# Performance work log

Measured on AMD Instinct MI355X. Metric: run time of the kernel, lower is better.

The kernel has to match this reference:

```python
import jax, jax.numpy as jnp
import numpy as np


def setup_inputs() -> dict:
    key = jax.random.key(0)
    k1, k2, k3, k4, k5, k6 = jax.random.split(key, 6)
    B, S, I, H = 64, 512, 1024, 1024
    scale_ih = 1.0 / np.sqrt(I)
    scale_hh = 1.0 / np.sqrt(H)
    return {
        "inputs": jax.random.normal(k1, (B, S, I), dtype=jnp.float32),
        "h0": jax.random.normal(k2, (1, B, H), dtype=jnp.float32),
        "weight_ih": jax.random.normal(k3, (H, I), dtype=jnp.float32) * scale_ih,
        "weight_hh": jax.random.normal(k4, (H, H), dtype=jnp.float32) * scale_hh,
        "bias_ih": jax.random.normal(k5, (H,), dtype=jnp.float32) * 0.01,
        "bias_hh": jax.random.normal(k6, (H,), dtype=jnp.float32) * 0.01,
    }


def reference(inputs, h0, weight_ih, weight_hh, bias_ih, bias_hh):
    # Elman RNN with ReLU: h_t = relu(x_t W_ih^T + b_ih + h_{t-1} W_hh^T + b_hh)
    # inputs: [B, S, I]; h0: [1, B, H]
    # Precompute the input projection for all timesteps in one big GEMM.
    x_proj = jnp.einsum('bsi,hi->bsh', inputs, weight_ih) + bias_ih + bias_hh  # [B,S,H]

    def step(h, xp_t):
        h_new = jax.nn.relu(xp_t + jnp.matmul(h, weight_hh.T))  # [B,H]
        return h_new, h_new

    h_init = h0[0]  # [B, H]
    h_last, outs = jax.lax.scan(step, h_init, jnp.swapaxes(x_proj, 0, 1))  # outs: [S,B,H]
    outputs = jnp.swapaxes(outs, 0, 1)  # [B, S, H]
    h_n = h_last[None]  # [1, B, H]
    return outputs, h_n
```

## Files before the change

kernel.cpp:

```cpp
#include <hip/hip_runtime.h>
#include <hip/hip_bf16.h>
#include <stdint.h>

#define BATCH 64
#define SEQ   512
#define INDIM 1024
#define HDIM  1024
#define NBLK  256
#define NGRP  8
#define GSLOT 32
#define FPAD  16
#define GBUF_U16 32768
#define GBUF_DW  16384

typedef short bf16x8 __attribute__((ext_vector_type(8)));
typedef short s16x4  __attribute__((ext_vector_type(4)));
typedef float f32x4  __attribute__((ext_vector_type(4)));
typedef unsigned short u16;
typedef unsigned int   u32;
typedef u32 u32x4 __attribute__((ext_vector_type(4)));
typedef u16 u16x4 __attribute__((ext_vector_type(4)));

static __device__ __forceinline__ u16 f2bf(float x) {
  unsigned int u = __float_as_uint(x);
  u += 0x7fffu + ((u >> 16) & 1u);
  return (u16)(u >> 16);
}
static __device__ __forceinline__ float bf2f(u16 b) {
  return __uint_as_float(((unsigned int)b) << 16);
}

static __device__ __forceinline__ int coh_ld_i32(const int* p) {
  int v;
  asm volatile("global_load_dword %0, %1, off sc0 sc1\n\t"
               "s_waitcnt vmcnt(0)"
               : "=&v"(v) : "v"(p) : "memory");
  return v;
}

static __device__ __forceinline__ void split4(float4 v, u16x4& hi, u16x4& lo) {
  hi.x = f2bf(v.x); lo.x = f2bf(v.x - bf2f(hi.x));
  hi.y = f2bf(v.y); lo.y = f2bf(v.y - bf2f(hi.y));
  hi.z = f2bf(v.z); lo.z = f2bf(v.z - bf2f(hi.z));
  hi.w = f2bf(v.w); lo.w = f2bf(v.w - bf2f(hi.w));
}
static __device__ __forceinline__ bf16x8 ld8(const u16* p) {
  s16x4 a = *(const s16x4*)p;
  s16x4 b = *(const s16x4*)(p + 4);
  return __builtin_shufflevector(a, b, 0, 1, 2, 3, 4, 5, 6, 7);
}

__global__ void init0(int* __restrict__ flags, int n) {
  int i = blockIdx.x * blockDim.x + threadIdx.x;
  if (i < n) flags[i] = 0;
}

__global__ void init1(const float* __restrict__ h0, u32* __restrict__ hw) {
  int i = blockIdx.x * blockDim.x + threadIdx.x;
  if (i < BATCH * HDIM) {
    int b = i >> 10, k = i & 1023;
    int g = b >> 3, r = b & 7;
    int k32 = k >> 5, kg = (k >> 3) & 3, j = k & 7;
    float x = h0[i];
    u16 hi = f2bf(x);
    u16 lo = f2bf(x - bf2f(hi));
    size_t di = (size_t)g * (2 * GBUF_DW) + (size_t)((k32 * 64 + kg * 16 + r) * 8 + j);
    hw[di] = (u32)hi | ((u32)lo << 16);
  }
}

__global__ __launch_bounds__(256) void xproj_kernel(const float* __restrict__ A,
                                                    const float* __restrict__ W,
                                                    const float* __restrict__ bih,
                                                    const float* __restrict__ bhh,
                                                    float* __restrict__ C) {
  __shared__ u16 Ah[4][128][12], Al[4][128][12], Bh[4][128][12], Bl[4][128][12];
  const int nb = blockIdx.x;
  const int mb = blockIdx.y;
  const int m_base = mb * 128, n_base = nb * 128;
  const int tid = (int)threadIdx.x;
  const int wid = tid >> 6, lane = tid & 63;
  const int wm = wid >> 1, wn = wid & 1;
  const int r = lane & 15, kg = lane >> 4;
  const int srow = tid >> 1;
  const int skq  = (tid & 1) * 16;

  const float* ap0 = A + (size_t)(m_base + srow) * INDIM + skq;
  const float* bp0 = W + (size_t)(n_base + srow) * INDIM + skq;

  f32x4 acc[4][4] = {};

  for (int k0 = 0; k0 < INDIM; k0 += 32) {
    float4 av[4], bv[4];
#pragma unroll
    for (int i = 0; i < 4; ++i) {
      av[i] = *(const float4*)(ap0 + k0 + i * 4);
      bv[i] = *(const float4*)(bp0 + k0 + i * 4);
    }
    __syncthreads();
#pragma unroll
    for (int i = 0; i < 4; ++i) {
      int kk = skq + i * 4;
      int kgw = kk >> 3, off = kk & 7;
      u16x4 hi, lo;
      split4(av[i], hi, lo);
      *(u16x4*)&Ah[kgw][srow][off] = hi;
      *(u16x4*)&Al[kgw][srow][off] = lo;
      split4(bv[i], hi, lo);
      *(u16x4*)&Bh[kgw][srow][off] = hi;
      *(u16x4*)&Bl[kgw][srow][off] = lo;
    }
    __syncthreads();

    bf16x8 ah[4], al[4], bhv[4], blv[4];
#pragma unroll
    for (int mf = 0; mf < 4; ++mf) {
      int row = wm * 64 + mf * 16 + r;
      ah[mf] = ld8(&Ah[kg][row][0]);
      al[mf] = ld8(&Al[kg][row][0]);
    }
#pragma unroll
    for (int nf = 0; nf < 4; ++nf) {
      int row = wn * 64 + nf * 16 + r;
      bhv[nf] = ld8(&Bh[kg][row][0]);
      blv[nf] = ld8(&Bl[kg][row][0]);
    }
#pragma unroll
    for (int mf = 0; mf < 4; ++mf)
#pragma unroll
      for (int nf = 0; nf < 4; ++nf) {
        acc[mf][nf] = __builtin_amdgcn_mfma_f32_16x16x32_bf16(ah[mf], bhv[nf], acc[mf][nf], 0, 0, 0);
        acc[mf][nf] = __builtin_amdgcn_mfma_f32_16x16x32_bf16(ah[mf], blv[nf], acc[mf][nf], 0, 0, 0);
        acc[mf][nf] = __builtin_amdgcn_mfma_f32_16x16x32_bf16(al[mf], bhv[nf], acc[mf][nf], 0, 0, 0);
      }
  }

#pragma unroll
  for (int nf = 0; nf < 4; ++nf) {
    int col = n_base + wn * 64 + nf * 16 + r;
    float bias = bih[col] + bhh[col];
#pragma unroll
    for (int mf = 0; mf < 4; ++mf) {
      int rowb = m_base + wm * 64 + mf * 16 + kg * 4;
#pragma unroll
      for (int q = 0; q < 4; ++q) {
        C[(size_t)(rowb + q) * HDIM + col] = acc[mf][nf][q] + bias;
      }
    }
  }
}

__global__ __launch_bounds__(576, 1) void rnn_scan(
    const float* __restrict__ Whh, float* __restrict__ out,
    u16* hbase, int* flags) {
  __shared__ u16 WH[32][2][64][8], WL[32][2][64][8];
  __shared__ __align__(16) float red[2][8][2][8][20];
  __shared__ __align__(16) float xfbuf[2][8][32];
  __shared__ __align__(16) float sbuf[2][8][32];

  const int blk = (int)blockIdx.x;
  const int grp = blk & 7;
  const int slot = blk >> 3;
  const int n0 = slot * 32;
  const int tid = (int)threadIdx.x;
  const int wv = tid >> 6, lane = tid & 63;
  const int r = lane & 15, kg = lane >> 4;
  const bool zrow = r >= 8;

  for (int f4 = tid; f4 < 8192; f4 += 576) {
    int row = f4 >> 8;
    int k0 = (f4 & 255) * 4;
    float4 v = *(const float4*)(Whh + (size_t)(n0 + row) * HDIM + k0);
    int k32 = k0 >> 5, kgg = (k0 >> 3) & 3, j = k0 & 7;
    int nt = row >> 4, ln = kgg * 16 + (row & 15);
    u16x4 hi, lo;
    split4(v, hi, lo);
    *(u16x4*)&WH[k32][nt][ln][j] = hi;
    *(u16x4*)&WL[k32][nt][ln][j] = lo;
  }
  __syncthreads();

  u16* const hb0 = hbase + (size_t)grp * (2 * GBUF_U16);
  u16* const hb1 = hb0 + GBUF_U16;
  int* const gflag = flags + grp * GSLOT * FPAD;
  const int* const pollp = gflag + ((wv & 7) * 4 + (lane & 3)) * FPAD;

  const int erow = lane >> 3;
  const int ec4 = (lane & 7) * 4;
  float* const xpp = out + ((size_t)(grp * 8 + erow) * SEQ) * HDIM + n0 + ec4;

  for (int t = 0; t < SEQ; ++t) {
    const int p2 = t & 1;

    if (wv < 8) {
      const u16* hc = (t & 1) ? hb1 : hb0;

      if (t > 0) {
        int v;
        do { v = coh_ld_i32(pollp); } while (!__all(v >= t));
      }

      u32x4 P0, P1, P2, P3, P4, P5, P6, P7;
      if (!zrow) {
        const char* a0 = (const char*)hc + (size_t)((wv * 4) * 64 + lane) * 32;
        const char* a1 = a0 + 4096;
        asm volatile(
            "global_load_dwordx4 %0, %8, off sc0 sc1\n\t"
            "global_load_dwordx4 %1, %8, off offset:16 sc0 sc1\n\t"
            "global_load_dwordx4 %2, %8, off offset:2048 sc0 sc1\n\t"
            "global_load_dwordx4 %3, %8, off offset:2064 sc0 sc1\n\t"
            "global_load_dwordx4 %4, %9, off sc0 sc1\n\t"
            "global_load_dwordx4 %5, %9, off offset:16 sc0 sc1\n\t"
            "global_load_dwordx4 %6, %9, off offset:2048 sc0 sc1\n\t"
            "global_load_dwordx4 %7, %9, off offset:2064 sc0 sc1"
            : "=&v"(P0), "=&v"(P1), "=&v"(P2), "=&v"(P3),
              "=&v"(P4), "=&v"(P5), "=&v"(P6), "=&v"(P7)
            : "v"(a0), "v"(a1)
            : "memory");
        asm volatile("s_waitcnt vmcnt(0)"
            : "+v"(P0), "+v"(P1), "+v"(P2), "+v"(P3),
              "+v"(P4), "+v"(P5), "+v"(P6), "+v"(P7));
      } else {
        P0 = P1 = P2 = P3 = P4 = P5 = P6 = P7 = (u32x4){0, 0, 0, 0};
      }

      f32x4 acc0 = {0.f, 0.f, 0.f, 0.f};
      f32x4 acc1 = {0.f, 0.f, 0.f, 0.f};
#define DO_K32(i, QA, QB)                                                      \
      {                                                                        \
        u32 d0 = QA[0], d1 = QA[1], d2 = QA[2], d3 = QA[3];                    \
        u32 d4 = QB[0], d5 = QB[1], d6 = QB[2], d7 = QB[3];                    \
        union { u32 w[4]; bf16x8 v; } AH, AL;                                  \
        AH.w[0] = (d0 & 0xFFFFu) | (d1 << 16);                                 \
        AH.w[1] = (d2 & 0xFFFFu) | (d3 << 16);                                 \
        AH.w[2] = (d4 & 0xFFFFu) | (d5 << 16);                                 \
        AH.w[3] = (d6 & 0xFFFFu) | (d7 << 16);                                 \
        AL.w[0] = (d0 >> 16) | (d1 & 0xFFFF0000u);                             \
        AL.w[1] = (d2 >> 16) | (d3 & 0xFFFF0000u);                             \
        AL.w[2] = (d4 >> 16) | (d5 & 0xFFFF0000u);                             \
        AL.w[3] = (d6 >> 16) | (d7 & 0xFFFF0000u);                             \
        int k32 = wv * 4 + (i);                                                \
        bf16x8 b0h = *(const bf16x8*)&WH[k32][0][lane][0];                     \
        bf16x8 b0l = *(const bf16x8*)&WL[k32][0][lane][0];                     \
        bf16x8 b1h = *(const bf16x8*)&WH[k32][1][lane][0];                     \
        bf16x8 b1l = *(const bf16x8*)&WL[k32][1][lane][0];                     \
        acc0 = __builtin_amdgcn_mfma_f32_16x16x32_bf16(AH.v, b0h, acc0, 0, 0, 0); \
        acc0 = __builtin_amdgcn_mfma_f32_16x16x32_bf16(AH.v, b0l, acc0, 0, 0, 0); \
        acc0 = __builtin_amdgcn_mfma_f32_16x16x32_bf16(AL.v, b0h, acc0, 0, 0, 0); \
        acc1 = __builtin_amdgcn_mfma_f32_16x16x32_bf16(AH.v, b1h, acc1, 0, 0, 0); \
        acc1 = __builtin_amdgcn_mfma_f32_16x16x32_bf16(AH.v, b1l, acc1, 0, 0, 0); \
        acc1 = __builtin_amdgcn_mfma_f32_16x16x32_bf16(AL.v, b1h, acc1, 0, 0, 0); \
      }
      DO_K32(0, P0, P1)
      DO_K32(1, P2, P3)
      DO_K32(2, P4, P5)
      DO_K32(3, P6, P7)
#undef DO_K32

      if (kg < 2) {
#pragma unroll
        for (int q = 0; q < 4; ++q) {
          red[p2][wv][0][kg * 4 + q][r] = acc0[q];
          red[p2][wv][1][kg * 4 + q][r] = acc1[q];
        }
      }
      __syncthreads();

      if (wv == 0) {
        f32x4 s = *(const f32x4*)&xfbuf[p2][erow][ec4];
        const int nt = ec4 >> 4, cl = ec4 & 15;
#pragma unroll
        for (int w = 0; w < 8; ++w) s += *(const f32x4*)&red[p2][w][nt][erow][cl];
#pragma unroll
        for (int j = 0; j < 4; ++j) s[j] = s[j] > 0.f ? s[j] : 0.f;
        *(f32x4*)&sbuf[p2][erow][ec4] = s;

        u32x4 D;
#pragma unroll
        for (int j = 0; j < 4; ++j) {
          u16 hi = f2bf(s[j]);
          u16 lo = f2bf(s[j] - bf2f(hi));
          D[j] = (u32)hi | ((u32)lo << 16);
        }
        u16* hnx = (t & 1) ? hb0 : hb1;
        u32* hp = (u32*)hnx + (size_t)((slot * 64 + (ec4 >> 3) * 16 + erow) * 8 + (ec4 & 7));
        asm volatile("global_store_dwordx4 %0, %1, off sc1\n\t"
                     "s_waitcnt vmcnt(0)"
                     :: "v"(hp), "v"(D) : "memory");
        if (lane == 0) {
          int* fp = gflag + slot * FPAD;
          int tv = t + 1;
          asm volatile("global_store_dword %0, %1, off sc0 sc1"
                       :: "v"(fp), "v"(tv) : "memory");
        }
      }
    } else {
      if (t >= 2) {
        f32x4 sv = *(const f32x4*)&sbuf[p2][erow][ec4];
        __builtin_nontemporal_store(sv, (f32x4*)(xpp + (size_t)(t - 2) * HDIM));
      }
      float4 xv = *(const float4*)(xpp + (size_t)t * HDIM);
      f32x4 xr = {xv.x, xv.y, xv.z, xv.w};
      *(f32x4*)&xfbuf[p2][erow][ec4] = xr;
      __syncthreads();
    }
  }

  __syncthreads();
  if (wv == 8) {
    f32x4 s2 = *(const f32x4*)&sbuf[(SEQ - 2) & 1][erow][ec4];
    __builtin_nontemporal_store(s2, (f32x4*)(xpp + (size_t)(SEQ - 2) * HDIM));
    f32x4 s1 = *(const f32x4*)&sbuf[(SEQ - 1) & 1][erow][ec4];
    __builtin_nontemporal_store(s1, (f32x4*)(xpp + (size_t)(SEQ - 1) * HDIM));
  }
}

__global__ void copy_hn(const float* __restrict__ out, float* __restrict__ hn) {
  int idx = blockIdx.x * blockDim.x + threadIdx.x;
  if (idx < BATCH * HDIM) {
    int b = idx >> 10, j = idx & 1023;
    hn[idx] = out[((size_t)b * SEQ + (SEQ - 1)) * (size_t)HDIM + j];
  }
}

extern "C" void kernel_launch(void* const* d_in, const int* in_sizes, int n_in,
                              void* d_out, int out_size, void* d_ws, size_t ws_size,
                              hipStream_t stream) {
  const float* inputs = (const float*)d_in[0];
  const float* h0     = (const float*)d_in[1];
  const float* w_ih   = (const float*)d_in[2];
  const float* w_hh   = (const float*)d_in[3];
  const float* b_ih   = (const float*)d_in[4];
  const float* b_hh   = (const float*)d_in[5];

  float* outBase = (float*)d_out;
  float* hnBase  = outBase + (size_t)BATCH * SEQ * HDIM;

  u16* hbase = (u16*)d_ws;
  int* flags = (int*)(hbase + (size_t)NGRP * 2 * GBUF_U16);
  const int nflags = NGRP * GSLOT * FPAD;

  init0<<<(nflags + 255) / 256, 256, 0, stream>>>(flags, nflags);
  init1<<<(BATCH * HDIM + 255) / 256, 256, 0, stream>>>(h0, (u32*)hbase);

  xproj_kernel<<<dim3(8, 256), 256, 0, stream>>>(inputs, w_ih, b_ih, b_hh, outBase);

  const float* wha = w_hh;
  float* oa = outBase;
  u16* hba = hbase;
  int* fa = flags;
  void* args[4] = {&wha, &oa, &hba, &fa};
  (void)hipLaunchCooperativeKernel((const void*)rnn_scan, dim3(NBLK), dim3(576), args, 0, stream);

  copy_hn<<<256, 256, 0, stream>>>(outBase, hnBase);
}
```

Baseline: 1.574 ms.

## Embed parity tags in hidden-state data to validate loads without a fence

Each bf16 hi word of the exchanged hidden state now carries a parity tag in its sign bit (XOR by a step-dependent mask). Consumers re-load until every element shows the expected tag, then XOR the tag away. This lets producers store without waiting on vmcnt, except at t=1. The epilogue also moves from wave 0 to wave 8, which holds the next x-proj value in a register and writes outputs directly, removing the xfbuf/sbuf staging and one barrier role. The flag poll is kept, so the tag check mainly covers data that arrives after its flag. The risk is extra re-load loops and subtle ordering bugs. The approach relies on the zrow padding and the initial 0xFFFF fill being consistent with the tag scheme.

```diff
diff --git a/kernel.cpp b/kernel.cpp
--- a/kernel.cpp
+++ b/kernel.cpp
@@ -50,9 +50,11 @@
   return __builtin_shufflevector(a, b, 0, 1, 2, 3, 4, 5, 6, 7);
 }
 
-__global__ void init0(int* __restrict__ flags, int n) {
+__global__ void init0(u32* __restrict__ ws) {
   int i = blockIdx.x * blockDim.x + threadIdx.x;
-  if (i < n) flags[i] = 0;
+  const int hdw = NGRP * 2 * GBUF_DW;
+  if (i < hdw) ws[i] = 0xFFFFFFFFu;
+  else if (i < hdw + NGRP * GSLOT * FPAD) ws[i] = 0;
 }
 
 __global__ void init1(const float* __restrict__ h0, u32* __restrict__ hw) {
@@ -155,8 +157,6 @@
     u16* hbase, int* flags) {
   __shared__ u16 WH[32][2][64][8], WL[32][2][64][8];
   __shared__ __align__(16) float red[2][8][2][8][20];
-  __shared__ __align__(16) float xfbuf[2][8][32];
-  __shared__ __align__(16) float sbuf[2][8][32];
 
   const int blk = (int)blockIdx.x;
   const int grp = blk & 7;
@@ -188,12 +188,19 @@
   const int erow = lane >> 3;
   const int ec4 = (lane & 7) * 4;
   float* const xpp = out + ((size_t)(grp * 8 + erow) * SEQ) * HDIM + n0 + ec4;
+  f32x4 xf = {0.f, 0.f, 0.f, 0.f};
+  if (wv == 8) {
+    float4 xv = *(const float4*)xpp;
+    xf = (f32x4){xv.x, xv.y, xv.z, xv.w};
+  }
 
   for (int t = 0; t < SEQ; ++t) {
     const int p2 = t & 1;
 
     if (wv < 8) {
       const u16* hc = (t & 1) ? hb1 : hb0;
+      const int rt = (t >> 1) & 1;
+      const u32 rm = rt ? 0x80008000u : 0u;
 
       if (t > 0) {
         int v;
@@ -204,22 +211,39 @@
       if (!zrow) {
         const char* a0 = (const char*)hc + (size_t)((wv * 4) * 64 + lane) * 32;
         const char* a1 = a0 + 4096;
-        asm volatile(
-            "global_load_dwordx4 %0, %8, off sc0 sc1\n\t"
-            "global_load_dwordx4 %1, %8, off offset:16 sc0 sc1\n\t"
-            "global_load_dwordx4 %2, %8, off offset:2048 sc0 sc1\n\t"
-            "global_load_dwordx4 %3, %8, off offset:2064 sc0 sc1\n\t"
-            "global_load_dwordx4 %4, %9, off sc0 sc1\n\t"
-            "global_load_dwordx4 %5, %9, off offset:16 sc0 sc1\n\t"
-            "global_load_dwordx4 %6, %9, off offset:2048 sc0 sc1\n\t"
-            "global_load_dwordx4 %7, %9, off offset:2064 sc0 sc1"
-            : "=&v"(P0), "=&v"(P1), "=&v"(P2), "=&v"(P3),
-              "=&v"(P4), "=&v"(P5), "=&v"(P6), "=&v"(P7)
-            : "v"(a0), "v"(a1)
-            : "memory");
-        asm volatile("s_waitcnt vmcnt(0)"
-            : "+v"(P0), "+v"(P1), "+v"(P2), "+v"(P3),
-              "+v"(P4), "+v"(P5), "+v"(P6), "+v"(P7));
+        for (;;) {
+          asm volatile(
+              "global_load_dwordx4 %0, %8, off sc0 sc1\n\t"
+              "global_load_dwordx4 %1, %8, off offset:16 sc0 sc1\n\t"
+              "global_load_dwordx4 %2, %8, off offset:2048 sc0 sc1\n\t"
+              "global_load_dwordx4 %3, %8, off offset:2064 sc0 sc1\n\t"
+              "global_load_dwordx4 %4, %9, off sc0 sc1\n\t"
+              "global_load_dwordx4 %5, %9, off offset:16 sc0 sc1\n\t"
+              "global_load_dwordx4 %6, %9, off offset:2048 sc0 sc1\n\t"
+              "global_load_dwordx4 %7, %9, off offset:2064 sc0 sc1"
+              : "=&v"(P0), "=&v"(P1), "=&v"(P2), "=&v"(P3),
+                "=&v"(P4), "=&v"(P5), "=&v"(P6), "=&v"(P7)
+              : "v"(a0), "v"(a1)
+              : "memory");
+          asm volatile("s_waitcnt vmcnt(0)"
+              : "+v"(P0), "+v"(P1), "+v"(P2), "+v"(P3),
+                "+v"(P4), "+v"(P5), "+v"(P6), "+v"(P7));
+          if (t == 0) break;
+          u32 m;
+          if (rt) {
+            m = P0[0] & P0[1] & P0[2] & P0[3] & P1[0] & P1[1] & P1[2] & P1[3]
+              & P2[0] & P2[1] & P2[2] & P2[3] & P3[0] & P3[1] & P3[2] & P3[3]
+              & P4[0] & P4[1] & P4[2] & P4[3] & P5[0] & P5[1] & P5[2] & P5[3]
+              & P6[0] & P6[1] & P6[2] & P6[3] & P7[0] & P7[1] & P7[2] & P7[3];
+          } else {
+            m = P0[0] | P0[1] | P0[2] | P0[3] | P1[0] | P1[1] | P1[2] | P1[3]
+              | P2[0] | P2[1] | P2[2] | P2[3] | P3[0] | P3[1] | P3[2] | P3[3]
+              | P4[0] | P4[1] | P4[2] | P4[3] | P5[0] | P5[1] | P5[2] | P5[3]
+              | P6[0] | P6[1] | P6[2] | P6[3] | P7[0] | P7[1] | P7[2] | P7[3];
+          }
+          bool ok = ((m >> 15) & 1u) == (u32)rt;
+          if (__all((int)ok)) break;
+        }
       } else {
         P0 = P1 = P2 = P3 = P4 = P5 = P6 = P7 = (u32x4){0, 0, 0, 0};
       }
@@ -231,10 +255,10 @@
         u32 d0 = QA[0], d1 = QA[1], d2 = QA[2], d3 = QA[3];                    \
         u32 d4 = QB[0], d5 = QB[1], d6 = QB[2], d7 = QB[3];                    \
         union { u32 w[4]; bf16x8 v; } AH, AL;                                  \
-        AH.w[0] = (d0 & 0xFFFFu) | (d1 << 16);                                 \
-        AH.w[1] = (d2 & 0xFFFFu) | (d3 << 16);                                 \
-        AH.w[2] = (d4 & 0xFFFFu) | (d5 << 16);                                 \
-        AH.w[3] = (d6 & 0xFFFFu) | (d7 << 16);                                 \
+        AH.w[0] = ((d0 & 0xFFFFu) | (d1 << 16)) ^ rm;                          \
+        AH.w[1] = ((d2 & 0xFFFFu) | (d3 << 16)) ^ rm;                          \
+        AH.w[2] = ((d4 & 0xFFFFu) | (d5 << 16)) ^ rm;                          \
+        AH.w[3] = ((d6 & 0xFFFFu) | (d7 << 16)) ^ rm;                          \
         AL.w[0] = (d0 >> 16) | (d1 & 0xFFFF0000u);                             \
         AL.w[1] = (d2 >> 16) | (d3 & 0xFFFF0000u);                             \
         AL.w[2] = (d4 >> 16) | (d5 & 0xFFFF0000u);                             \
@@ -265,53 +289,45 @@
         }
       }
       __syncthreads();
-
-      if (wv == 0) {
-        f32x4 s = *(const f32x4*)&xfbuf[p2][erow][ec4];
-        const int nt = ec4 >> 4, cl = ec4 & 15;
-#pragma unroll
-        for (int w = 0; w < 8; ++w) s += *(const f32x4*)&red[p2][w][nt][erow][cl];
-#pragma unroll
-        for (int j = 0; j < 4; ++j) s[j] = s[j] > 0.f ? s[j] : 0.f;
-        *(f32x4*)&sbuf[p2][erow][ec4] = s;
-
-        u32x4 D;
-#pragma unroll
-        for (int j = 0; j < 4; ++j) {
-          u16 hi = f2bf(s[j]);
-          u16 lo = f2bf(s[j] - bf2f(hi));
-          D[j] = (u32)hi | ((u32)lo << 16);
-        }
-        u16* hnx = (t & 1) ? hb0 : hb1;
-        u32* hp = (u32*)hnx + (size_t)((slot * 64 + (ec4 >> 3) * 16 + erow) * 8 + (ec4 & 7));
+    } else {
+      __syncthreads();
+      f32x4 s = xf;
+      const int nt = ec4 >> 4, cl = ec4 & 15;
+#pragma unroll
+      for (int w = 0; w < 8; ++w) s += *(const f32x4*)&red[p2][w][nt][erow][cl];
+#pragma unroll
+      for (int j = 0; j < 4; ++j) s[j] = s[j] > 0.f ? s[j] : 0.f;
+
+      const u16 wtag = (u16)((((t + 1) >> 1) & 1) << 15);
+      u32x4 D;
+#pragma unroll
+      for (int j = 0; j < 4; ++j) {
+        u16 hi = f2bf(s[j]);
+        u16 lo = f2bf(s[j] - bf2f(hi));
+        D[j] = (u32)(u16)(hi ^ wtag) | ((u32)lo << 16);
+      }
+      u16* hnx = (t & 1) ? hb0 : hb1;
+      u32* hp = (u32*)hnx + (size_t)((slot * 64 + (ec4 >> 3) * 16 + erow) * 8 + (ec4 & 7));
+      if (t == 1) {
         asm volatile("global_store_dwordx4 %0, %1, off sc1\n\t"
                      "s_waitcnt vmcnt(0)"
                      :: "v"(hp), "v"(D) : "memory");
-        if (lane == 0) {
-          int* fp = gflag + slot * FPAD;
-          int tv = t + 1;
-          asm volatile("global_store_dword %0, %1, off sc0 sc1"
-                       :: "v"(fp), "v"(tv) : "memory");
-        }
-      }
-    } else {
-      if (t >= 2) {
-        f32x4 sv = *(const f32x4*)&sbuf[p2][erow][ec4];
-        __builtin_nontemporal_store(sv, (f32x4*)(xpp + (size_t)(t - 2) * HDIM));
-      }
-      float4 xv = *(const float4*)(xpp + (size_t)t * HDIM);
-      f32x4 xr = {xv.x, xv.y, xv.z, xv.w};
-      *(f32x4*)&xfbuf[p2][erow][ec4] = xr;
-      __syncthreads();
-    }
-  }
-
-  __syncthreads();
-  if (wv == 8) {
-    f32x4 s2 = *(const f32x4*)&sbuf[(SEQ - 2) & 1][erow][ec4];
-    __builtin_nontemporal_store(s2, (f32x4*)(xpp + (size_t)(SEQ - 2) * HDIM));
-    f32x4 s1 = *(const f32x4*)&sbuf[(SEQ - 1) & 1][erow][ec4];
-    __builtin_nontemporal_store(s1, (f32x4*)(xpp + (size_t)(SEQ - 1) * HDIM));
+      } else {
+        asm volatile("global_store_dwordx4 %0, %1, off sc1"
+                     :: "v"(hp), "v"(D) : "memory");
+      }
+      if (lane == 0) {
+        int* fp = gflag + slot * FPAD;
+        int tv = t + 1;
+        asm volatile("global_store_dword %0, %1, off sc0 sc1"
+                     :: "v"(fp), "v"(tv) : "memory");
+      }
+      __builtin_nontemporal_store(s, (f32x4*)(xpp + (size_t)t * HDIM));
+      if (t + 1 < SEQ) {
+        float4 xv = *(const float4*)(xpp + (size_t)(t + 1) * HDIM);
+        xf = (f32x4){xv.x, xv.y, xv.z, xv.w};
+      }
+    }
   }
 }
 
@@ -338,9 +354,9 @@
 
   u16* hbase = (u16*)d_ws;
   int* flags = (int*)(hbase + (size_t)NGRP * 2 * GBUF_U16);
-  const int nflags = NGRP * GSLOT * FPAD;
-
-  init0<<<(nflags + 255) / 256, 256, 0, stream>>>(flags, nflags);
+
+  const int init_n = NGRP * 2 * GBUF_DW + NGRP * GSLOT * FPAD;
+  init0<<<(init_n + 255) / 256, 256, 0, stream>>>((u32*)d_ws);
   init1<<<(BATCH * HDIM + 255) / 256, 256, 0, stream>>>(h0, (u32*)hbase);
 
   xproj_kernel<<<dim3(8, 256), 256, 0, stream>>>(inputs, w_ih, b_ih, b_hh, outBase);
```

Result: no change. 1.602 ms (+1.8%).
